# Optimization experiments

Measured on AMD Instinct MI355X. Metric: run time of the kernel, lower is better.

## Reference

```python
import jax, jax.numpy as jnp
import numpy as np

N, E, D, C = 10000, 320000, 128, 3  # nodes, edges, hidden/feat dim, coord dim


def _lin_init(key, fan_in, fan_out, bias=True):
    k1, k2 = jax.random.split(key)
    bound = 1.0 / np.sqrt(fan_in)
    W = jax.random.uniform(k1, (fan_in, fan_out), jnp.float32, -bound, bound)
    if bias:
        b = jax.random.uniform(k2, (fan_out,), jnp.float32, -bound, bound)
        return W, b
    return W


def setup_inputs() -> dict:
    key = jax.random.key(0)
    ks = jax.random.split(key, 12)
    h = jax.random.normal(ks[0], (N, D), jnp.float32)
    coord = jax.random.normal(ks[1], (N, C), jnp.float32)
    edge_index = jax.random.randint(ks[2], (2, E), 0, N, jnp.int64)
    We1, be1 = _lin_init(ks[3], 2 * D + 1, D)   # edge_mlp layer 1
    We2, be2 = _lin_init(ks[4], D, D)           # edge_mlp layer 2
    Wa, ba = _lin_init(ks[5], D, 1)             # att_mlp
    Wn1, bn1 = _lin_init(ks[6], D + D, D)       # node_mlp layer 1
    Wn2, bn2 = _lin_init(ks[7], D, D)           # node_mlp layer 2
    Wc1, bc1 = _lin_init(ks[8], D, D)           # coord_mlp layer 1
    Wc2 = _lin_init(ks[9], D, 1, bias=False)    # coord_mlp layer 2 (no bias)
    return dict(h=h, edge_index=edge_index, coord=coord,
                We1=We1, be1=be1, We2=We2, be2=be2, Wa=Wa, ba=ba,
                Wn1=Wn1, bn1=bn1, Wn2=Wn2, bn2=bn2, Wc1=Wc1, bc1=bc1, Wc2=Wc2)


def reference(h, edge_index, coord, We1, be1, We2, be2, Wa, ba,
              Wn1, bn1, Wn2, bn2, Wc1, bc1, Wc2):
    row, col = edge_index[0], edge_index[1]
    # coord2radial (normalize=False)
    coord_diff = coord[row] - coord[col]                      # [E, 3]
    radial = jnp.sum(coord_diff ** 2, axis=1, keepdims=True)  # [E, 1]
    # edge_model: cat(source, target, radial) -> MLP -> attention gate
    e_in = jnp.concatenate([h[row], h[col], radial], axis=1)  # [E, 2D+1]
    m = jax.nn.silu(e_in @ We1 + be1)
    m = jax.nn.silu(m @ We2 + be2)                            # [E, D]
    att = jax.nn.sigmoid(m @ Wa + ba)                         # [E, 1]
    edge_feat = m * att                                       # [E, D]
    # coord_model: scatter-mean of gated coord diffs
    w = jax.nn.silu(edge_feat @ Wc1 + bc1) @ Wc2              # [E, 1]
    trans = coord_diff * w                                    # [E, 3]
    agg_c = jax.ops.segment_sum(trans, row, num_segments=N)
    cnt = jax.ops.segment_sum(jnp.ones((E,), jnp.float32), row, num_segments=N)
    coord_out = coord + agg_c / jnp.maximum(cnt, 1.0)[:, None]
    # node_model: scatter-sum of edge features, residual MLP
    agg_h = jax.ops.segment_sum(edge_feat, row, num_segments=N)  # [N, D]
    n_in = jnp.concatenate([h, agg_h], axis=1)
    out = jax.nn.silu(n_in @ Wn1 + bn1) @ Wn2 + bn2
    h_out = h + out  # residual=True
    return h_out, coord_out
```

## Files before the change

### kernel.cpp

```cpp
#include <hip/hip_runtime.h>
#include <hip/hip_bf16.h>

#define NN 10000
#define EE 320000
#define DD 128
#define TEE 128

typedef __attribute__((ext_vector_type(8))) __bf16 bf16x8;
typedef __attribute__((ext_vector_type(2))) __bf16 bf16x2;
typedef __attribute__((ext_vector_type(8))) unsigned short ushort8;
typedef __attribute__((ext_vector_type(4))) float  f32x4;

__device__ __forceinline__ float silu_f(float x) {
    return x * __builtin_amdgcn_rcpf(1.0f + __expf(-x));
}
__device__ __forceinline__ float sigmoid_f(float x) {
    return __builtin_amdgcn_rcpf(1.0f + __expf(-x));
}
__device__ __forceinline__ unsigned pkbf(float a, float b) {
    bf16x2 v; v.x = (__bf16)a; v.y = (__bf16)b;
    return __builtin_bit_cast(unsigned, v);
}
__device__ __forceinline__ unsigned short sbf(float a) {
    return __builtin_bit_cast(unsigned short, (__bf16)a);
}
__device__ __forceinline__ float bf2f(unsigned short u) {
    return __builtin_bit_cast(float, (unsigned)u << 16);
}
__device__ __forceinline__ float atomic_add_f(float* p, float v) {
    return unsafeAtomicAdd(p, v);
}

__global__ __launch_bounds__(256)
void front_kernel(const int* __restrict__ ei, int* __restrict__ cnt,
                  const float* __restrict__ We1, const float* __restrict__ We2,
                  const float* __restrict__ Wc1, const float* __restrict__ Wn1,
                  const float* __restrict__ Wn2, unsigned short* __restrict__ pW,
                  float* __restrict__ aggz)
{
    const int b = blockIdx.x;
    const int tid = threadIdx.x;
    if (b < 313) {
        const int t4 = b * 256 + tid;
        if (t4 < EE / 4) {
            const int4 e4 = *(const int4*)&ei[t4 * 4];
            atomicAdd(&cnt[e4.x], 1);
            atomicAdd(&cnt[e4.y], 1);
            atomicAdd(&cnt[e4.z], 1);
            atomicAdd(&cnt[e4.w], 1);
        }
    } else if (b < 761) {
        const int idx = (b - 313) * 256 + tid;
        const float* src; int loc, nks, koff = 0;
        if (idx < 16384)       { src = We1; loc = idx;         nks = 4; }
        else if (idx < 32768)  { src = We1; loc = idx - 16384; nks = 4; koff = 128; }
        else if (idx < 49152)  { src = We2; loc = idx - 32768; nks = 4; }
        else if (idx < 65536)  { src = Wc1; loc = idx - 49152; nks = 4; }
        else if (idx < 98304)  { src = Wn1; loc = idx - 65536; nks = 8; }
        else                   { src = Wn2; loc = idx - 98304; nks = 4; }
        const int per_ct = nks * 512;
        const int ct = loc / per_ct;
        const int r  = loc % per_ct;
        const int ks = r >> 9;
        const int r2 = r & 511;
        const int ln = r2 >> 3;
        const int j  = r2 & 7;
        const int k  = ks * 32 + (ln >> 4) * 8 + j + koff;
        const int n  = ct * 16 + (ln & 15);
        pW[idx] = sbf(src[k * DD + n]);
    } else {
        const int base = ((b - 761) * 256 + tid) * 4;
        float4* p = (float4*)aggz;
#pragma unroll
        for (int k = 0; k < 4; ++k) {
            const int i = base + k;
            if (i < 327500) p[i] = make_float4(0.f, 0.f, 0.f, 0.f);
        }
    }
}

__global__ __launch_bounds__(1024)
void scan_kernel(const int* __restrict__ cnt, int* __restrict__ offs)
{
    __shared__ int wsum[16];
    const int t = threadIdx.x;
    const int lane = t & 63;
    const int wv = t >> 6;
    const int base = t * 10;
    int loc[10];
    int s = 0;
#pragma unroll
    for (int i = 0; i < 10; ++i) {
        const int idx = base + i;
        const int v = (idx < NN) ? cnt[idx] : 0;
        loc[i] = s; s += v;
    }
    int ps = s;
#pragma unroll
    for (int d = 1; d < 64; d <<= 1) {
        const int u = __shfl_up(ps, d);
        if (lane >= d) ps += u;
    }
    if (lane == 63) wsum[wv] = ps;
    __syncthreads();
    if (wv == 0 && lane < 16) {
        int v = wsum[lane];
#pragma unroll
        for (int d = 1; d < 16; d <<= 1) {
            const int u = __shfl_up(v, d, 16);
            if ((lane & 15) >= d) v += u;
        }
        wsum[lane] = v;
    }
    __syncthreads();
    const int wbase = (wv == 0) ? 0 : wsum[wv - 1];
    const int pre = wbase + ps - s;
#pragma unroll
    for (int i = 0; i < 10; ++i) {
        const int idx = base + i;
        if (idx < NN) offs[idx] = pre + loc[i];
    }
    if (t == 1023) offs[NN] = wbase + ps;
}

__global__ __launch_bounds__(256, 2)
void mid_kernel(const int* __restrict__ ei, const int* __restrict__ offs,
                int* __restrict__ tmp, int2* __restrict__ eidx,
                const float* __restrict__ h, const float* __restrict__ be1,
                const unsigned short* __restrict__ pW,
                unsigned short* __restrict__ P, unsigned short* __restrict__ Q)
{
    const int b = blockIdx.x;
    const int tid = threadIdx.x;
    if (b < 1250) {
        const int e = b * 256 + tid;
        if (e < EE) {
            const int r = ei[e];
            const int c = ei[EE + e];
            const int pos = offs[r] + atomicAdd(&tmp[r], 1);
            eidx[pos] = make_int2(r, c);
        }
        return;
    }
    __shared__ __align__(16) unsigned short sAbuf[32 * 128];
    const int w    = tid >> 6;
    const int lane = tid & 63;
    const int g    = lane >> 4;
    const int l15  = lane & 15;
    const int n0   = (b - 1250) * 32;
    char* const sAb = (char*)sAbuf;

#pragma unroll
    for (int i = 0; i < 2; ++i) {
        const int idx = tid * 2 + i;
        const int row = idx >> 4, c = idx & 15;
        const int n = n0 + row;
        float4 a = make_float4(0.f, 0.f, 0.f, 0.f);
        float4 bb = make_float4(0.f, 0.f, 0.f, 0.f);
        if (n < NN) {
            a  = *(const float4*)&h[(size_t)n * DD + c * 8];
            bb = *(const float4*)&h[(size_t)n * DD + c * 8 + 4];
        }
        uint4 pk;
        pk.x = pkbf(a.x, a.y);  pk.y = pkbf(a.z, a.w);
        pk.z = pkbf(bb.x, bb.y); pk.w = pkbf(bb.z, bb.w);
        *(uint4*)(sAb + row * 256 + ((c * 16) ^ ((row & 7) << 4))) = pk;
    }
    __syncthreads();

    f32x4 accP[2][2], accQ[2][2];
    {
        float be1c[2];
#pragma unroll
        for (int ctl = 0; ctl < 2; ++ctl)
            be1c[ctl] = be1[w * 32 + ctl * 16 + l15];
#pragma unroll
        for (int rt = 0; rt < 2; ++rt)
#pragma unroll
            for (int ctl = 0; ctl < 2; ++ctl)
#pragma unroll
                for (int j = 0; j < 4; ++j) {
                    accP[rt][ctl][j] = be1c[ctl];
                    accQ[rt][ctl][j] = 0.f;
                }
    }
    const unsigned short* pWa = pW;
    const unsigned short* pWb = pW + 16384;
#pragma unroll 1
    for (int ks = 0; ks < 4; ++ks) {
        bf16x8 a[2];
#pragma unroll
        for (int rt = 0; rt < 2; ++rt) {
            const int row = rt * 16 + l15;
            const int byc = g * 16 + ks * 64;
            a[rt] = *(const bf16x8*)(sAb + row * 256 + (byc ^ ((row & 7) << 4)));
        }
        const bf16x8 pa0 = *(const bf16x8*)&pWa[(((2 * w + 0) * 4 + ks) * 64 + lane) * 8];
        const bf16x8 pa1 = *(const bf16x8*)&pWa[(((2 * w + 1) * 4 + ks) * 64 + lane) * 8];
        const bf16x8 pb0 = *(const bf16x8*)&pWb[(((2 * w + 0) * 4 + ks) * 64 + lane) * 8];
        const bf16x8 pb1 = *(const bf16x8*)&pWb[(((2 * w + 1) * 4 + ks) * 64 + lane) * 8];
#pragma unroll
        for (int rt = 0; rt < 2; ++rt) {
            accP[rt][0] = __builtin_amdgcn_mfma_f32_16x16x32_bf16(a[rt], pa0, accP[rt][0], 0, 0, 0);
            accP[rt][1] = __builtin_amdgcn_mfma_f32_16x16x32_bf16(a[rt], pa1, accP[rt][1], 0, 0, 0);
            accQ[rt][0] = __builtin_amdgcn_mfma_f32_16x16x32_bf16(a[rt], pb0, accQ[rt][0], 0, 0, 0);
            accQ[rt][1] = __builtin_amdgcn_mfma_f32_16x16x32_bf16(a[rt], pb1, accQ[rt][1], 0, 0, 0);
        }
    }
#pragma unroll
    for (int rt = 0; rt < 2; ++rt)
#pragma unroll
        for (int ctl = 0; ctl < 2; ++ctl)
#pragma unroll
            for (int j = 0; j < 4; ++j) {
                const int row = rt * 16 + g * 4 + j;
                const int n = n0 + row;
                if (n < NN) {
                    const int col = w * 32 + ctl * 16 + l15;
                    P[(size_t)n * DD + col] = sbf(accP[rt][ctl][j]);
                    Q[(size_t)n * DD + col] = sbf(accQ[rt][ctl][j]);
                }
            }
}

__global__ __launch_bounds__(512, 6)
void edge_kernel(const int2* __restrict__ eidx,
                 const float* __restrict__ coord,
                 const unsigned short* __restrict__ P, const unsigned short* __restrict__ Q,
                 const float* __restrict__ We1,
                 const float* __restrict__ be2,
                 const float* __restrict__ Wa, const float* __restrict__ ba,
                 const float* __restrict__ bc1, const float* __restrict__ Wc2,
                 const unsigned short* __restrict__ pW,
                 float* __restrict__ agg_h, float* __restrict__ agg_c)
{
    __shared__ __align__(16) unsigned short sM[128 * 128];
    __shared__ __align__(16) float sWred[4][128];
    __shared__ __align__(16) int   sRow[128];
    __shared__ int   sCol[128];
    __shared__ __align__(16) float sRad[128];
    __shared__ __align__(16) float sAtt[128];
    __shared__ float sCd[128][3];

    const int tid  = threadIdx.x;
    const int w    = tid >> 6;
    const int lane = tid & 63;
    const int g    = lane >> 4;
    const int l15  = lane & 15;
    const int rh   = w >> 2;
    const int cq   = w & 3;
    const int rb   = rh * 64;
    const int e0g  = blockIdx.x * TEE;
    char* const sMb = (char*)sM;

    if (tid < TEE) {
        const int2 rc = eidx[e0g + tid];
        sRow[tid] = rc.x; sCol[tid] = rc.y;
        const float dx = coord[rc.x * 3 + 0] - coord[rc.y * 3 + 0];
        const float dy = coord[rc.x * 3 + 1] - coord[rc.y * 3 + 1];
        const float dz = coord[rc.x * 3 + 2] - coord[rc.y * 3 + 2];
        sCd[tid][0] = dx; sCd[tid][1] = dy; sCd[tid][2] = dz;
        sRad[tid] = dx * dx + dy * dy + dz * dz;
    }
    __syncthreads();

    {
        const int el  = tid >> 2;
        const int sub = tid & 3;
        const int rg = sRow[el], cg = sCol[el];
        const float rad = sRad[el];
        const unsigned short* Prow = P + (size_t)rg * DD;
        const unsigned short* Qrow = Q + (size_t)cg * DD;
        const float* We1r = We1 + 256 * DD;
#pragma unroll
        for (int i = 0; i < 4; ++i) {
            const int c8 = sub * 4 + i;
            const ushort8 pu = __builtin_bit_cast(ushort8, *(const bf16x8*)&Prow[c8 * 8]);
            const ushort8 qu = __builtin_bit_cast(ushort8, *(const bf16x8*)&Qrow[c8 * 8]);
            const float4 w0 = *(const float4*)&We1r[c8 * 8];
            const float4 w1 = *(const float4*)&We1r[c8 * 8 + 4];
            float x[8];
            x[0] = fmaf(rad, w0.x, bf2f(pu[0]) + bf2f(qu[0]));
            x[1] = fmaf(rad, w0.y, bf2f(pu[1]) + bf2f(qu[1]));
            x[2] = fmaf(rad, w0.z, bf2f(pu[2]) + bf2f(qu[2]));
            x[3] = fmaf(rad, w0.w, bf2f(pu[3]) + bf2f(qu[3]));
            x[4] = fmaf(rad, w1.x, bf2f(pu[4]) + bf2f(qu[4]));
            x[5] = fmaf(rad, w1.y, bf2f(pu[5]) + bf2f(qu[5]));
            x[6] = fmaf(rad, w1.z, bf2f(pu[6]) + bf2f(qu[6]));
            x[7] = fmaf(rad, w1.w, bf2f(pu[7]) + bf2f(qu[7]));
            uint4 pk;
            pk.x = pkbf(silu_f(x[0]), silu_f(x[1]));
            pk.y = pkbf(silu_f(x[2]), silu_f(x[3]));
            pk.z = pkbf(silu_f(x[4]), silu_f(x[5]));
            pk.w = pkbf(silu_f(x[6]), silu_f(x[7]));
            *(uint4*)(sMb + el * 256 + ((c8 * 16) ^ ((el & 7) << 4))) = pk;
        }
    }
    __syncthreads();

    f32x4 acc[4][2];

    {
        float be2c[2];
#pragma unroll
        for (int ctl = 0; ctl < 2; ++ctl)
            be2c[ctl] = be2[cq * 32 + ctl * 16 + l15];
#pragma unroll
        for (int rt = 0; rt < 4; ++rt)
#pragma unroll
            for (int ctl = 0; ctl < 2; ++ctl)
#pragma unroll
                for (int j = 0; j < 4; ++j)
                    acc[rt][ctl][j] = be2c[ctl];
        const unsigned short* pWe2 = pW + 32768;
#pragma unroll 1
        for (int ks = 0; ks < 4; ++ks) {
            bf16x8 a[4];
#pragma unroll
            for (int rt = 0; rt < 4; ++rt) {
                const int row = rb + rt * 16 + l15;
                const int byc = g * 16 + ks * 64;
                a[rt] = *(const bf16x8*)(sMb + row * 256 + (byc ^ ((row & 7) << 4)));
            }
            const bf16x8 b0 = *(const bf16x8*)&pWe2[(((2 * cq + 0) * 4 + ks) * 64 + lane) * 8];
            const bf16x8 b1 = *(const bf16x8*)&pWe2[(((2 * cq + 1) * 4 + ks) * 64 + lane) * 8];
#pragma unroll
            for (int rt = 0; rt < 4; ++rt) {
                acc[rt][0] = __builtin_amdgcn_mfma_f32_16x16x32_bf16(a[rt], b0, acc[rt][0], 0, 0, 0);
                acc[rt][1] = __builtin_amdgcn_mfma_f32_16x16x32_bf16(a[rt], b1, acc[rt][1], 0, 0, 0);
            }
        }
    }
#pragma unroll
    for (int rt = 0; rt < 4; ++rt)
#pragma unroll
        for (int ctl = 0; ctl < 2; ++ctl)
#pragma unroll
            for (int j = 0; j < 4; ++j)
                acc[rt][ctl][j] = silu_f(acc[rt][ctl][j]);

    {
        float wac[2];
#pragma unroll
        for (int ctl = 0; ctl < 2; ++ctl)
            wac[ctl] = Wa[cq * 32 + ctl * 16 + l15];
        float part[4][4];
#pragma unroll
        for (int rt = 0; rt < 4; ++rt)
#pragma unroll
            for (int j = 0; j < 4; ++j)
                part[rt][j] = fmaf(acc[rt][0][j], wac[0], acc[rt][1][j] * wac[1]);
#pragma unroll
        for (int msk = 1; msk < 16; msk <<= 1)
#pragma unroll
            for (int rt = 0; rt < 4; ++rt)
#pragma unroll
                for (int j = 0; j < 4; ++j)
                    part[rt][j] += __shfl_xor(part[rt][j], msk);
        if (l15 == 0) {
#pragma unroll
            for (int rt = 0; rt < 4; ++rt) {
                float4 p4 = make_float4(part[rt][0], part[rt][1], part[rt][2], part[rt][3]);
                *(float4*)&sWred[cq][rb + rt * 16 + g * 4] = p4;
            }
        }
    }
    __syncthreads();
    if (tid < TEE) {
        const float s = sWred[0][tid] + sWred[1][tid] + sWred[2][tid] + sWred[3][tid];
        sAtt[tid] = sigmoid_f(s + ba[0]);
    }
    __syncthreads();

#pragma unroll
    for (int rt = 0; rt < 4; ++rt) {
        const float4 a4 = *(const float4*)&sAtt[rb + rt * 16 + g * 4];
        const float at[4] = {a4.x, a4.y, a4.z, a4.w};
#pragma unroll
        for (int ctl = 0; ctl < 2; ++ctl) {
            const int col = cq * 32 + ctl * 16 + l15;
#pragma unroll
            for (int j = 0; j < 4; ++j) {
                const float v = acc[rt][ctl][j] * at[j];
                const int row = rb + rt * 16 + g * 4 + j;
                *(unsigned short*)(sMb + row * 256 + ((col * 2) ^ ((row & 7) << 4))) = sbf(v);
            }
        }
    }
    __syncthreads();

    {
        float bc1c[2];
#pragma unroll
        for (int ctl = 0; ctl < 2; ++ctl)
            bc1c[ctl] = bc1[cq * 32 + ctl * 16 + l15];
#pragma unroll
        for (int rt = 0; rt < 4; ++rt)
#pragma unroll
            for (int ctl = 0; ctl < 2; ++ctl)
#pragma unroll
                for (int j = 0; j < 4; ++j)
                    acc[rt][ctl][j] = bc1c[ctl];
        const unsigned short* pWc1 = pW + 49152;
#pragma unroll 1
        for (int ks = 0; ks < 4; ++ks) {
            bf16x8 a[4];
#pragma unroll
            for (int rt = 0; rt < 4; ++rt) {
                const int row = rb + rt * 16 + l15;
                const int byc = g * 16 + ks * 64;
                a[rt] = *(const bf16x8*)(sMb + row * 256 + (byc ^ ((row & 7) << 4)));
            }
            const bf16x8 b0 = *(const bf16x8*)&pWc1[(((2 * cq + 0) * 4 + ks) * 64 + lane) * 8];
            const bf16x8 b1 = *(const bf16x8*)&pWc1[(((2 * cq + 1) * 4 + ks) * 64 + lane) * 8];
#pragma unroll
            for (int rt = 0; rt < 4; ++rt) {
                acc[rt][0] = __builtin_amdgcn_mfma_f32_16x16x32_bf16(a[rt], b0, acc[rt][0], 0, 0, 0);
                acc[rt][1] = __builtin_amdgcn_mfma_f32_16x16x32_bf16(a[rt], b1, acc[rt][1], 0, 0, 0);
            }
        }
        float wcc[2];
#pragma unroll
        for (int ctl = 0; ctl < 2; ++ctl)
            wcc[ctl] = Wc2[cq * 32 + ctl * 16 + l15];
        float part[4][4];
#pragma unroll
        for (int rt = 0; rt < 4; ++rt)
#pragma unroll
            for (int j = 0; j < 4; ++j)
                part[rt][j] = fmaf(silu_f(acc[rt][0][j]), wcc[0], silu_f(acc[rt][1][j]) * wcc[1]);
#pragma unroll
        for (int msk = 1; msk < 16; msk <<= 1)
#pragma unroll
            for (int rt = 0; rt < 4; ++rt)
#pragma unroll
                for (int j = 0; j < 4; ++j)
                    part[rt][j] += __shfl_xor(part[rt][j], msk);
        if (l15 == 0) {
#pragma unroll
            for (int rt = 0; rt < 4; ++rt) {
                float4 p4 = make_float4(part[rt][0], part[rt][1], part[rt][2], part[rt][3]);
                *(float4*)&sWred[cq][rb + rt * 16 + g * 4] = p4;
            }
        }
    }
    __syncthreads();

    {
        const int col = tid & 127;
        const int seg = tid >> 7;
        const int ebeg = seg * 32;
        float a = 0.f;
        int cur = sRow[ebeg];
#pragma unroll 1
        for (int e = ebeg; e < ebeg + 32; ++e) {
            const int r = sRow[e];
            if (r != cur) {
                atomic_add_f(&agg_h[(size_t)cur * DD + col], a);
                a = 0.f; cur = r;
            }
            const unsigned short u =
                *(const unsigned short*)(sMb + e * 256 + ((col * 2) ^ ((e & 7) << 4)));
            a += bf2f(u);
        }
        atomic_add_f(&agg_h[(size_t)cur * DD + col], a);
    }

    if (tid < 12) {
        const int c = tid % 3;
        const int seg = tid / 3;
        const int ebeg = seg * 32;
        float a = 0.f;
        int cur = sRow[ebeg];
#pragma unroll 1
        for (int e = ebeg; e < ebeg + 32; ++e) {
            const int r = sRow[e];
            if (r != cur) {
                atomic_add_f(&agg_c[cur * 3 + c], a);
                a = 0.f; cur = r;
            }
            const float wv = sWred[0][e] + sWred[1][e] + sWred[2][e] + sWred[3][e];
            a += sCd[e][c] * wv;
        }
        atomic_add_f(&agg_c[cur * 3 + c], a);
    }
}

__global__ __launch_bounds__(256, 2)
void node_kernel(const float* __restrict__ h, const float* __restrict__ coord,
                 const float* __restrict__ bn1, const float* __restrict__ bn2,
                 const unsigned short* __restrict__ pW,
                 const float* __restrict__ agg_h, const float* __restrict__ agg_c,
                 const int* __restrict__ cnt,
                 float* __restrict__ hout, float* __restrict__ cout)
{
    __shared__ __align__(16) unsigned short sAbuf[32 * 256];

    const int tid  = threadIdx.x;
    const int w    = tid >> 6;
    const int lane = tid & 63;
    const int g    = lane >> 4;
    const int l15  = lane & 15;
    const int n0   = blockIdx.x * 32;
    char* const sAb = (char*)sAbuf;

    {
        const int halfsel = (lane >= 32) ? 1 : 0;
        const int bytec   = (lane & 31) * 8 + halfsel * 256;
        const float* src  = halfsel ? agg_h : h;
#pragma unroll 4
        for (int s = 0; s < 8; ++s) {
            const int row = w * 8 + s;
            const int n = n0 + row;
            float4 v = make_float4(0.f, 0.f, 0.f, 0.f);
            if (n < NN) v = *(const float4*)&src[(size_t)n * DD + (lane & 31) * 4];
            uint2 pk;
            pk.x = pkbf(v.x, v.y);
            pk.y = pkbf(v.z, v.w);
            *(uint2*)(sAb + row * 512 + (bytec ^ ((row & 7) << 4))) = pk;
        }
    }
    __syncthreads();

    f32x4 acc[2][2];

    {
        float bc[2];
#pragma unroll
        for (int ctl = 0; ctl < 2; ++ctl)
            bc[ctl] = bn1[w * 32 + ctl * 16 + l15];
#pragma unroll
        for (int rt = 0; rt < 2; ++rt)
#pragma unroll
            for (int ctl = 0; ctl < 2; ++ctl)
#pragma unroll
                for (int j = 0; j < 4; ++j)
                    acc[rt][ctl][j] = bc[ctl];
        const unsigned short* pWn1 = pW + 65536;
#pragma unroll 1
        for (int ks = 0; ks < 8; ++ks) {
            bf16x8 a[2];
#pragma unroll
            for (int rt = 0; rt < 2; ++rt) {
                const int row = rt * 16 + l15;
                const int byc = g * 16 + ks * 64;
                a[rt] = *(const bf16x8*)(sAb + row * 512 + (byc ^ ((row & 7) << 4)));
            }
            const bf16x8 b0 = *(const bf16x8*)&pWn1[(((2 * w + 0) * 8 + ks) * 64 + lane) * 8];
            const bf16x8 b1 = *(const bf16x8*)&pWn1[(((2 * w + 1) * 8 + ks) * 64 + lane) * 8];
#pragma unroll
            for (int rt = 0; rt < 2; ++rt) {
                acc[rt][0] = __builtin_amdgcn_mfma_f32_16x16x32_bf16(a[rt], b0, acc[rt][0], 0, 0, 0);
                acc[rt][1] = __builtin_amdgcn_mfma_f32_16x16x32_bf16(a[rt], b1, acc[rt][1], 0, 0, 0);
            }
        }
    }
    __syncthreads();
#pragma unroll
    for (int rt = 0; rt < 2; ++rt)
#pragma unroll
        for (int ctl = 0; ctl < 2; ++ctl)
#pragma unroll
            for (int j = 0; j < 4; ++j) {
                const int row = rt * 16 + g * 4 + j;
                const int col = w * 32 + ctl * 16 + l15;
                *(unsigned short*)(sAb + row * 256 + ((col * 2) ^ ((row & 7) << 4)))
                    = sbf(silu_f(acc[rt][ctl][j]));
            }
    __syncthreads();

    {
        float bc[2];
#pragma unroll
        for (int ctl = 0; ctl < 2; ++ctl)
            bc[ctl] = bn2[w * 32 + ctl * 16 + l15];
#pragma unroll
        for (int rt = 0; rt < 2; ++rt)
#pragma unroll
            for (int ctl = 0; ctl < 2; ++ctl)
#pragma unroll
                for (int j = 0; j < 4; ++j)
                    acc[rt][ctl][j] = bc[ctl];
        const unsigned short* pWn2 = pW + 98304;
#pragma unroll 1
        for (int ks = 0; ks < 4; ++ks) {
            bf16x8 a[2];
#pragma unroll
            for (int rt = 0; rt < 2; ++rt) {
                const int row = rt * 16 + l15;
                const int byc = g * 16 + ks * 64;
                a[rt] = *(const bf16x8*)(sAb + row * 256 + (byc ^ ((row & 7) << 4)));
            }
            const bf16x8 b0 = *(const bf16x8*)&pWn2[(((2 * w + 0) * 4 + ks) * 64 + lane) * 8];
            const bf16x8 b1 = *(const bf16x8*)&pWn2[(((2 * w + 1) * 4 + ks) * 64 + lane) * 8];
#pragma unroll
            for (int rt = 0; rt < 2; ++rt) {
                acc[rt][0] = __builtin_amdgcn_mfma_f32_16x16x32_bf16(a[rt], b0, acc[rt][0], 0, 0, 0);
                acc[rt][1] = __builtin_amdgcn_mfma_f32_16x16x32_bf16(a[rt], b1, acc[rt][1], 0, 0, 0);
            }
        }
    }
#pragma unroll
    for (int rt = 0; rt < 2; ++rt)
#pragma unroll
        for (int ctl = 0; ctl < 2; ++ctl)
#pragma unroll
            for (int j = 0; j < 4; ++j) {
                const int row = rt * 16 + g * 4 + j;
                const int n = n0 + row;
                if (n < NN) {
                    const int col = w * 32 + ctl * 16 + l15;
                    hout[(size_t)n * DD + col] = h[(size_t)n * DD + col] + acc[rt][ctl][j];
                }
            }

    if (tid < 96) {
        const int e = tid / 3, c = tid % 3;
        const int n = n0 + e;
        if (n < NN) {
            const float cn = fmaxf((float)cnt[n], 1.0f);
            cout[n * 3 + c] = coord[n * 3 + c] + agg_c[n * 3 + c] / cn;
        }
    }
}

extern "C" void kernel_launch(void* const* d_in, const int* in_sizes, int n_in,
                              void* d_out, int out_size, void* d_ws, size_t ws_size,
                              hipStream_t stream)
{
    const float* h     = (const float*)d_in[0];
    const int*   ei    = (const int*)  d_in[1];
    const float* coord = (const float*)d_in[2];
    const float* We1   = (const float*)d_in[3];
    const float* be1   = (const float*)d_in[4];
    const float* We2   = (const float*)d_in[5];
    const float* be2   = (const float*)d_in[6];
    const float* Wa    = (const float*)d_in[7];
    const float* ba    = (const float*)d_in[8];
    const float* Wn1   = (const float*)d_in[9];
    const float* bn1   = (const float*)d_in[10];
    const float* Wn2   = (const float*)d_in[11];
    const float* bn2   = (const float*)d_in[12];
    const float* Wc1   = (const float*)d_in[13];
    const float* bc1   = (const float*)d_in[14];
    const float* Wc2   = (const float*)d_in[15];

    float* agg_h   = (float*)d_ws;
    float* agg_c   = agg_h + (size_t)NN * DD;
    int*   cnt_i   = (int*)(agg_c + (size_t)NN * 3);
    int*   tmp_i   = cnt_i + NN;
    int*   offs    = tmp_i + NN;
    int2*  eidx    = (int2*)(offs + 10016);
    unsigned short* pW = (unsigned short*)(eidx + EE);
    unsigned short* P  = pW + 114688;
    unsigned short* Q  = P + (size_t)NN * DD;

    (void)hipMemsetAsync(cnt_i, 0, (size_t)(2 * NN) * sizeof(int), stream);

    front_kernel<<<1081, 256, 0, stream>>>(ei, cnt_i, We1, We2, Wc1, Wn1, Wn2,
                                           pW, agg_h);
    scan_kernel<<<1, 1024, 0, stream>>>(cnt_i, offs);
    mid_kernel<<<1563, 256, 0, stream>>>(ei, offs, tmp_i, eidx, h, be1, pW, P, Q);

    edge_kernel<<<EE / TEE, 512, 0, stream>>>(eidx, coord, P, Q, We1, be2,
                                              Wa, ba, bc1, Wc2, pW, agg_h, agg_c);

    float* hout = (float*)d_out;
    float* cout = hout + (size_t)NN * DD;
    node_kernel<<<313, 256, 0, stream>>>(h, coord, bn1, bn2, pW,
                                         agg_h, agg_c, cnt_i, hout, cout);
}
```

Before: 187.3 us.

## Double edge tile to 256 with 1024-thread blocks; replace scan with atomic offset allocation

The edge kernel now processes 256 edges per block with 1024 threads, doubling every shared-memory buffer, so weight staging and per-block setup are spread over more edges. The single-block prefix scan is replaced by a 40-block kernel in which each node reserves its edge range with an atomicAdd on a global counter. Rows stay contiguous in the edge list but are no longer placed in node order. The launch bound of 1024 threads with a minimum of 8 blocks per multiprocessor may force register spills in the edge kernel, and the larger LDS footprint lowers how many blocks can be resident at once.

```diff
diff --git a/kernel.cpp b/kernel.cpp
--- a/kernel.cpp
+++ b/kernel.cpp
@@ -4,7 +4,7 @@
 #define NN 10000
 #define EE 320000
 #define DD 128
-#define TEE 128
+#define TEE 256
 
 typedef __attribute__((ext_vector_type(8))) __bf16 bf16x8;
 typedef __attribute__((ext_vector_type(2))) __bf16 bf16x2;
@@ -79,48 +79,12 @@
     }
 }
 
-__global__ __launch_bounds__(1024)
-void scan_kernel(const int* __restrict__ cnt, int* __restrict__ offs)
+__global__ __launch_bounds__(256)
+void alloc_kernel(const int* __restrict__ cnt, int* __restrict__ offs,
+                  int* __restrict__ ctr)
 {
-    __shared__ int wsum[16];
-    const int t = threadIdx.x;
-    const int lane = t & 63;
-    const int wv = t >> 6;
-    const int base = t * 10;
-    int loc[10];
-    int s = 0;
-#pragma unroll
-    for (int i = 0; i < 10; ++i) {
-        const int idx = base + i;
-        const int v = (idx < NN) ? cnt[idx] : 0;
-        loc[i] = s; s += v;
-    }
-    int ps = s;
-#pragma unroll
-    for (int d = 1; d < 64; d <<= 1) {
-        const int u = __shfl_up(ps, d);
-        if (lane >= d) ps += u;
-    }
-    if (lane == 63) wsum[wv] = ps;
-    __syncthreads();
-    if (wv == 0 && lane < 16) {
-        int v = wsum[lane];
-#pragma unroll
-        for (int d = 1; d < 16; d <<= 1) {
-            const int u = __shfl_up(v, d, 16);
-            if ((lane & 15) >= d) v += u;
-        }
-        wsum[lane] = v;
-    }
-    __syncthreads();
-    const int wbase = (wv == 0) ? 0 : wsum[wv - 1];
-    const int pre = wbase + ps - s;
-#pragma unroll
-    for (int i = 0; i < 10; ++i) {
-        const int idx = base + i;
-        if (idx < NN) offs[idx] = pre + loc[i];
-    }
-    if (t == 1023) offs[NN] = wbase + ps;
+    const int n = blockIdx.x * 256 + threadIdx.x;
+    if (n < NN) offs[n] = atomicAdd(ctr, cnt[n]);
 }
 
 __global__ __launch_bounds__(256, 2)
@@ -223,7 +187,7 @@
             }
 }
 
-__global__ __launch_bounds__(512, 6)
+__global__ __launch_bounds__(1024, 8)
 void edge_kernel(const int2* __restrict__ eidx,
                  const float* __restrict__ coord,
                  const unsigned short* __restrict__ P, const unsigned short* __restrict__ Q,
@@ -234,13 +198,13 @@
                  const unsigned short* __restrict__ pW,
                  float* __restrict__ agg_h, float* __restrict__ agg_c)
 {
-    __shared__ __align__(16) unsigned short sM[128 * 128];
-    __shared__ __align__(16) float sWred[4][128];
-    __shared__ __align__(16) int   sRow[128];
-    __shared__ int   sCol[128];
-    __shared__ __align__(16) float sRad[128];
-    __shared__ __align__(16) float sAtt[128];
-    __shared__ float sCd[128][3];
+    __shared__ __align__(16) unsigned short sM[256 * 128];
+    __shared__ __align__(16) float sWred[4][256];
+    __shared__ __align__(16) int   sRow[256];
+    __shared__ int   sCol[256];
+    __shared__ __align__(16) float sRad[256];
+    __shared__ __align__(16) float sAtt[256];
+    __shared__ float sCd[256][3];
 
     const int tid  = threadIdx.x;
     const int w    = tid >> 6;
@@ -466,7 +430,7 @@
         atomic_add_f(&agg_h[(size_t)cur * DD + col], a);
     }
 
-    if (tid < 12) {
+    if (tid < 24) {
         const int c = tid % 3;
         const int seg = tid / 3;
         const int ebeg = seg * 32;
@@ -654,16 +618,17 @@
     unsigned short* pW = (unsigned short*)(eidx + EE);
     unsigned short* P  = pW + 114688;
     unsigned short* Q  = P + (size_t)NN * DD;
-
-    (void)hipMemsetAsync(cnt_i, 0, (size_t)(2 * NN) * sizeof(int), stream);
+    int* ctr = offs + 10008;
+
+    (void)hipMemsetAsync(cnt_i, 0, (size_t)(2 * NN + 10016) * sizeof(int), stream);
 
     front_kernel<<<1081, 256, 0, stream>>>(ei, cnt_i, We1, We2, Wc1, Wn1, Wn2,
                                            pW, agg_h);
-    scan_kernel<<<1, 1024, 0, stream>>>(cnt_i, offs);
+    alloc_kernel<<<40, 256, 0, stream>>>(cnt_i, offs, ctr);
     mid_kernel<<<1563, 256, 0, stream>>>(ei, offs, tmp_i, eidx, h, be1, pW, P, Q);
 
-    edge_kernel<<<EE / TEE, 512, 0, stream>>>(eidx, coord, P, Q, We1, be2,
-                                              Wa, ba, bc1, Wc2, pW, agg_h, agg_c);
+    edge_kernel<<<EE / TEE, 1024, 0, stream>>>(eidx, coord, P, Q, We1, be2,
+                                               Wa, ba, bc1, Wc2, pW, agg_h, agg_c);
 
     float* hout = (float*)d_out;
     float* cout = hout + (size_t)NN * DD;
```

After: 200.7 us. 7.1% more time.
